# Kernel optimization log

Measured on AMD Instinct MI355X. Metric: run time of the kernel, lower is better.

The kernel has to match this reference:

```python
import jax, jax.numpy as jnp
import numpy as np

N = 8192      # number of nodes
D = 16        # inp_dim (forced by W: [16,18])
DH = 18       # GAT hidden dim (forced by W/a)
H = 8         # num_heads


def setup_inputs() -> dict:
    key = jax.random.key(0)
    k1, k2, k3, k4 = jax.random.split(key, 4)
    inputs = jax.random.normal(k1, (N, D), dtype=jnp.float32)
    # xavier-ish init scale for W (torch uses xavier_uniform gain=1.414)
    W = jax.random.normal(k2, (D, DH), dtype=jnp.float32) * np.float32(np.sqrt(2.0 / (D + DH)) * 1.414)
    a = jax.random.normal(k3, (2 * DH, 1), dtype=jnp.float32) * np.float32(0.1)
    Wk = jax.random.normal(k4, (H, D, D), dtype=jnp.float32)  # stacked attention_wts_k
    return {"inputs": inputs, "W": W, "a": a, "Wk": Wk}


def reference(inputs, W, a, Wk):
    # h = inputs @ W  -> [N, 18]
    h = jnp.matmul(inputs, W)
    # a_input[i, j] = concat(h[i], h[j]); score e[i,j] = a_input[i,j] @ a.
    # Decompose instead of materializing [N*N, 36]:
    #   e[i,j] = h[i] @ a[:18] + h[j] @ a[18:]
    a1 = a[:DH, 0]  # [18]
    a2 = a[DH:, 0]  # [18]
    e = (h @ a1)[:, None] + (h @ a2)[None, :]        # [N, N]
    # softmax over dim=-2 of [N, N, 1] == axis 1 of [N, N] (neighbor axis)
    score = jax.nn.softmax(e, axis=1)                # [N, N]
    # per-head linear: op1[h] = inputs @ Wk[h]  -> [H, N, 16]
    op1 = jnp.einsum('nd,hde->hne', inputs, Wk)
    # scored_x sum over neighbors: out[i,h,:] = sum_j score[i,j] * op1[h,j,:]
    out = jnp.einsum('nm,hmd->nhd', score, op1)      # [N, H, 16]
    return out.reshape(N, H * D)                     # concat heads -> [N, 128]
```

## Files before the change

### kernel.cpp

```cpp
#include <hip/hip_runtime.h>
#include <hip/hip_bf16.h>

#define N 8192
#define D 16
#define DH 18
#define H 8
#define NBLK_A 32


__global__ void attn_partial(const float* __restrict__ x, const float* __restrict__ W,
                             const float* __restrict__ a, float* __restrict__ ws) {
    __shared__ float w2[D];
    __shared__ float part[4][D + 1];
    int t = threadIdx.x;
    if (t < D) {
        float acc = 0.f;
        #pragma unroll
        for (int j = 0; j < DH; ++j) acc += W[t * DH + j] * a[DH + j];
        w2[t] = acc;
    }
    __syncthreads();

    int m = blockIdx.x * blockDim.x + t;
    const float4* xp = reinterpret_cast<const float4*>(x + (size_t)m * D);
    float4 q0 = xp[0], q1 = xp[1], q2 = xp[2], q3 = xp[3];
    float xv[D];
    xv[0]=q0.x; xv[1]=q0.y; xv[2]=q0.z; xv[3]=q0.w;
    xv[4]=q1.x; xv[5]=q1.y; xv[6]=q1.z; xv[7]=q1.w;
    xv[8]=q2.x; xv[9]=q2.y; xv[10]=q2.z; xv[11]=q2.w;
    xv[12]=q3.x; xv[13]=q3.y; xv[14]=q3.z; xv[15]=q3.w;

    float g = 0.f;
    #pragma unroll
    for (int d = 0; d < D; ++d) g += xv[d] * w2[d];
    float w = expf(g);

    float acc[D + 1];
    acc[0] = w;
    #pragma unroll
    for (int d = 0; d < D; ++d) acc[1 + d] = w * xv[d];

    #pragma unroll
    for (int off = 32; off > 0; off >>= 1) {
        #pragma unroll
        for (int k = 0; k < D + 1; ++k)
            acc[k] += __shfl_down(acc[k], off, 64);
    }
    int wave = t >> 6, lane = t & 63;
    if (lane == 0) {
        #pragma unroll
        for (int k = 0; k < D + 1; ++k) part[wave][k] = acc[k];
    }
    __syncthreads();
    if (t < D + 1) {
        float s = part[0][t] + part[1][t] + part[2][t] + part[3][t];
        ws[t * NBLK_A + blockIdx.x] = s;
    }
}

__global__ void attn_write(const float* __restrict__ Wk, const float* __restrict__ ws,
                           float* __restrict__ out) {
    __shared__ float sv[D + 1];
    __shared__ float ov[H * D];
    int t = threadIdx.x;
    if (t < D + 1) {
        float s = 0.f;
        #pragma unroll
        for (int b = 0; b < NBLK_A; ++b) s += ws[t * NBLK_A + b];
        sv[t] = s;
    }
    __syncthreads();
    if (t < H * D) {
        int h = t >> 4, e = t & 15;
        float inv = 1.0f / sv[0];
        float acc = 0.f;
        #pragma unroll
        for (int d = 0; d < D; ++d)
            acc += sv[1 + d] * Wk[h * (D * D) + d * D + e];
        ov[t] = acc * inv;
    }
    __syncthreads();

    const float4* ov4 = reinterpret_cast<const float4*>(ov);
    float4* out4 = reinterpret_cast<float4*>(out);
    const int total = N * (H * D / 4);
    for (int idx = blockIdx.x * blockDim.x + t; idx < total; idx += gridDim.x * blockDim.x) {
        out4[idx] = ov4[idx & 31];
    }
}

extern "C" void kernel_launch(void* const* d_in, const int* in_sizes, int n_in,
                              void* d_out, int out_size, void* d_ws, size_t ws_size,
                              hipStream_t stream) {
    const float* inputs = (const float*)d_in[0];
    const float* W      = (const float*)d_in[1];
    const float* a      = (const float*)d_in[2];
    const float* Wk     = (const float*)d_in[3];
    float* out = (float*)d_out;
    float* ws  = (float*)d_ws;

    attn_partial<<<NBLK_A, 256, 0, stream>>>(inputs, W, a, ws);
    attn_write<<<256, 256, 0, stream>>>(Wk, ws, out);
}
```

Baseline: 63.42 us.

## Fuse partial reduction and broadcast write into one kernel with redundant per-block reduction

Merges the two kernels into a single launch. Each of 64 blocks of 1024 threads redundantly reduces all 8192 rows to the softmax-weighted sum of x, then computes the 128-wide output vector and writes its own slice of the broadcast output. This removes the second launch and the workspace round trip. The cost is that every block rereads the full 512KB input, which should mostly hit in cache.

```diff
diff --git a/kernel.cpp b/kernel.cpp
--- a/kernel.cpp
+++ b/kernel.cpp
@@ -5,14 +5,23 @@
 #define D 16
 #define DH 18
 #define H 8
-#define NBLK_A 32
+#define NB 64
+#define BT 1024
+#define ROWS_PER_T (N / BT)
+#define F4_TOTAL (N * H * D / 4)
+#define F4_PER_BLK (F4_TOTAL / NB)
+#define F4_PER_T (F4_PER_BLK / BT)
 
+__global__ __launch_bounds__(BT) void attn_fused(
+        const float* __restrict__ x, const float* __restrict__ W,
+        const float* __restrict__ a, const float* __restrict__ Wk,
+        float* __restrict__ out) {
+    __shared__ float w2[D];
+    __shared__ float part[BT / 64][D + 1];
+    __shared__ float sv[D + 1];
+    __shared__ float ov[H * D];
+    int t = threadIdx.x;
 
-__global__ void attn_partial(const float* __restrict__ x, const float* __restrict__ W,
-                             const float* __restrict__ a, float* __restrict__ ws) {
-    __shared__ float w2[D];
-    __shared__ float part[4][D + 1];
-    int t = threadIdx.x;
     if (t < D) {
         float acc = 0.f;
         #pragma unroll
@@ -21,24 +30,34 @@
     }
     __syncthreads();
 
-    int m = blockIdx.x * blockDim.x + t;
-    const float4* xp = reinterpret_cast<const float4*>(x + (size_t)m * D);
-    float4 q0 = xp[0], q1 = xp[1], q2 = xp[2], q3 = xp[3];
-    float xv[D];
-    xv[0]=q0.x; xv[1]=q0.y; xv[2]=q0.z; xv[3]=q0.w;
-    xv[4]=q1.x; xv[5]=q1.y; xv[6]=q1.z; xv[7]=q1.w;
-    xv[8]=q2.x; xv[9]=q2.y; xv[10]=q2.z; xv[11]=q2.w;
-    xv[12]=q3.x; xv[13]=q3.y; xv[14]=q3.z; xv[15]=q3.w;
-
-    float g = 0.f;
+    float w2r[D];
     #pragma unroll
-    for (int d = 0; d < D; ++d) g += xv[d] * w2[d];
-    float w = expf(g);
+    for (int d = 0; d < D; ++d) w2r[d] = w2[d];
 
     float acc[D + 1];
-    acc[0] = w;
     #pragma unroll
-    for (int d = 0; d < D; ++d) acc[1 + d] = w * xv[d];
+    for (int k = 0; k < D + 1; ++k) acc[k] = 0.f;
+
+    #pragma unroll
+    for (int r = 0; r < ROWS_PER_T; ++r) {
+        int m = r * BT + t;
+        const float4* xp = reinterpret_cast<const float4*>(x + (size_t)m * D);
+        float4 q0 = xp[0], q1 = xp[1], q2 = xp[2], q3 = xp[3];
+        float xv[D];
+        xv[0]=q0.x; xv[1]=q0.y; xv[2]=q0.z; xv[3]=q0.w;
+        xv[4]=q1.x; xv[5]=q1.y; xv[6]=q1.z; xv[7]=q1.w;
+        xv[8]=q2.x; xv[9]=q2.y; xv[10]=q2.z; xv[11]=q2.w;
+        xv[12]=q3.x; xv[13]=q3.y; xv[14]=q3.z; xv[15]=q3.w;
+
+        float g = 0.f;
+        #pragma unroll
+        for (int d = 0; d < D; ++d) g += xv[d] * w2r[d];
+        float w = expf(g);
+
+        acc[0] += w;
+        #pragma unroll
+        for (int d = 0; d < D; ++d) acc[1 + d] += w * xv[d];
+    }
 
     #pragma unroll
     for (int off = 32; off > 0; off >>= 1) {
@@ -53,40 +72,28 @@
     }
     __syncthreads();
     if (t < D + 1) {
-        float s = part[0][t] + part[1][t] + part[2][t] + part[3][t];
-        ws[t * NBLK_A + blockIdx.x] = s;
-    }
-}
-
-__global__ void attn_write(const float* __restrict__ Wk, const float* __restrict__ ws,
-                           float* __restrict__ out) {
-    __shared__ float sv[D + 1];
-    __shared__ float ov[H * D];
-    int t = threadIdx.x;
-    if (t < D + 1) {
         float s = 0.f;
         #pragma unroll
-        for (int b = 0; b < NBLK_A; ++b) s += ws[t * NBLK_A + b];
+        for (int wv = 0; wv < BT / 64; ++wv) s += part[wv][t];
         sv[t] = s;
     }
     __syncthreads();
     if (t < H * D) {
         int h = t >> 4, e = t & 15;
         float inv = 1.0f / sv[0];
-        float acc = 0.f;
+        float o = 0.f;
         #pragma unroll
         for (int d = 0; d < D; ++d)
-            acc += sv[1 + d] * Wk[h * (D * D) + d * D + e];
-        ov[t] = acc * inv;
+            o += sv[1 + d] * Wk[h * (D * D) + d * D + e];
+        ov[t] = o * inv;
     }
     __syncthreads();
 
-    const float4* ov4 = reinterpret_cast<const float4*>(ov);
-    float4* out4 = reinterpret_cast<float4*>(out);
-    const int total = N * (H * D / 4);
-    for (int idx = blockIdx.x * blockDim.x + t; idx < total; idx += gridDim.x * blockDim.x) {
-        out4[idx] = ov4[idx & 31];
-    }
+    float4 myv = reinterpret_cast<const float4*>(ov)[t & 31];
+    float4* out4 = reinterpret_cast<float4*>(out) + (size_t)blockIdx.x * F4_PER_BLK;
+    #pragma unroll
+    for (int i = 0; i < F4_PER_T; ++i)
+        out4[i * BT + t] = myv;
 }
 
 extern "C" void kernel_launch(void* const* d_in, const int* in_sizes, int n_in,
@@ -97,8 +104,6 @@
     const float* a      = (const float*)d_in[2];
     const float* Wk     = (const float*)d_in[3];
     float* out = (float*)d_out;
-    float* ws  = (float*)d_ws;
 
-    attn_partial<<<NBLK_A, 256, 0, stream>>>(inputs, W, a, ws);
-    attn_write<<<256, 256, 0, stream>>>(Wk, ws, out);
+    attn_fused<<<NB, BT, 0, stream>>>(inputs, W, a, Wk, out);
 }
```

New measurement: 99.95 us. 57.6% more time.
